# Optimization experiments

Measured on AMD Instinct MI355X. Metric: run time of the kernel, lower is better.

## Reference

```python
import jax, jax.numpy as jnp
import numpy as np

IN_D = 512
VOCAB = 32000
SEQ = 2048

def setup_inputs() -> dict:
    key = jax.random.key(0)
    ks = jax.random.split(key, 12)
    d = IN_D
    def xavier(k, shape):
        fan_in, fan_out = shape[1], shape[0]
        a = jnp.sqrt(6.0 / (fan_in + fan_out))
        return jax.random.uniform(k, shape, jnp.float32, -a, a)
    return {
        'X': jax.random.randint(ks[0], (1, SEQ), 0, VOCAB),
        'wz': xavier(ks[1], (VOCAB, d)),
        'uz': xavier(ks[2], (d, d)),
        'w': xavier(ks[3], (VOCAB, d)),
        'u': xavier(ks[4], (d, d)),
        'wr': xavier(ks[5], (VOCAB, d)),
        'ur': xavier(ks[6], (d, d)),
        'wy': xavier(ks[7], (VOCAB, d)),
        'bz': xavier(ks[8], (1, d)),
        'br': xavier(ks[9], (1, d)),
        'bh': xavier(ks[10], (1, d)),
        'by': xavier(ks[11], (1, VOCAB)),
    }

def reference(X, wz, uz, w, u, wr, ur, wy, bz, br, bh, by):
    idx = X[0]                      # (T,) batch is hardcoded to 1 in original
    ez = wz[idx]                    # (T, d) per-step embedding gathers, done once
    er = wr[idx]
    eh = w[idx]

    def step(h, emb):
        e_z, e_r, e_h = emb
        z = jax.nn.sigmoid(e_z + h @ uz.T + bz[0])
        r = jax.nn.sigmoid(e_r + h @ ur.T + br[0])
        h_xh = jnp.tanh(e_h + (r * h) @ u.T + bh[0])
        h_new = h * z + (1.0 - z) * h_xh
        return h_new, h_new

    h0 = jnp.zeros((wz.shape[1],), dtype=wz.dtype)
    _, hs = jax.lax.scan(step, h0, (ez, er, eh))   # hs: (T, d)
    logits = hs @ wy.T + by[0]                     # (T, vocab)
    outs = jax.nn.log_softmax(logits, axis=-1)     # matches squeeze(0)
    hiddens = hs[None, :, :]                       # (1, T, d)
    return outs, hiddens
```

## Files before the change

### kernel.cpp

```cpp
#include <hip/hip_runtime.h>
#include <math.h>

typedef unsigned short u16;
typedef unsigned long long u64;
typedef unsigned short us8 __attribute__((ext_vector_type(8)));
typedef short bf16x8 __attribute__((ext_vector_type(8)));
typedef float f32x4 __attribute__((ext_vector_type(4)));

#define D       512
#define SEQ     2048
#define VOCAB   32000
#define NB      16
#define RPB     32
#define STPB    512
#define PBSTR   576
#define PBTOT   (2 * NB * PBSTR)

__device__ __forceinline__ u16 f2bf(float f) {
    union { float f; unsigned i; } x; x.f = f;
    unsigned r = x.i + 0x7fff + ((x.i >> 16) & 1);
    return (u16)(r >> 16);
}

__device__ __forceinline__ u64 tag_ld(const u64* p) {
    return __hip_atomic_load(p, __ATOMIC_RELAXED, __HIP_MEMORY_SCOPE_AGENT);
}
__device__ __forceinline__ void tag_st(u64* p, u64 v) {
    __hip_atomic_store(p, v, __ATOMIC_RELAXED, __HIP_MEMORY_SCOPE_AGENT);
}
__device__ __forceinline__ u64 packtv(float f, unsigned tag) {
    union { float f; unsigned i; } x; x.f = f;
    return ((u64)tag << 32) | (u64)x.i;
}
__device__ __forceinline__ float unpackv(u64 v) {
    union { unsigned i; float f; } x; x.i = (unsigned)v;
    return x.f;
}
__device__ __forceinline__ float ftanh(float x) {
    return 1.f - 2.f / (1.f + __expf(2.f * x));
}
__device__ __forceinline__ void bar_lds() {
    asm volatile("s_waitcnt lgkmcnt(0)" ::: "memory");
    __builtin_amdgcn_s_barrier();
}

__global__ void init_scratch(u64* __restrict__ pbuf)
{
    const int t = blockIdx.x * blockDim.x + threadIdx.x;
    if (t < PBTOT) pbuf[t] = 0ull;
}

__global__ __launch_bounds__(STPB, 2) void scan_kernel(
    const int* __restrict__ X,
    const float* __restrict__ WZ, const float* __restrict__ UZ,
    const float* __restrict__ W,  const float* __restrict__ U,
    const float* __restrict__ WR, const float* __restrict__ UR,
    const float* __restrict__ BZ, const float* __restrict__ BR,
    const float* __restrict__ BH,
    u64* __restrict__ pbuf,
    float* __restrict__ outH)
{
    __shared__ int   idxsm[SEQ];
    __shared__ float hsm[(D / 32) * 33];
    __shared__ float rhsm[RPB];

    const int tid = threadIdx.x, b = blockIdx.x;
    const int r  = tid >> 4;
    const int cg = tid & 15;
    const int c0 = cg * 32;
    const int g  = b * RPB + r;
    const int i  = tid;

    for (int k = tid; k < SEQ; k += STPB) idxsm[k] = X[k];

    float uzw[32], urw[32], ucol[32];
#pragma unroll
    for (int j = 0; j < 32; j += 4) {
        f32x4 vz = *(const f32x4*)&UZ[(size_t)g * D + c0 + j];
        f32x4 vr = *(const f32x4*)&UR[(size_t)g * D + c0 + j];
        f32x4 vu = *(const f32x4*)&U [(size_t)i * D + b * RPB + j];
#pragma unroll
        for (int q = 0; q < 4; ++q) {
            uzw[j + q]  = vz[q];
            urw[j + q]  = vr[q];
            ucol[j + q] = vu[q];
        }
    }
    const float bzv = BZ[g], brv = BR[g], bhv = BH[i];

    hsm[(i >> 5) * 33 + (i & 31)] = 0.f;
    __syncthreads();

    const int i0 = idxsm[0];
    float ezc = WZ[(size_t)i0 * D + g];
    float erc = WR[(size_t)i0 * D + g];
    float ehc = W [(size_t)i0 * D + i];

    float hprev = 0.f;
    u64* const pb0 = pbuf;
    u64* const pb1 = pbuf + NB * PBSTR;

#pragma unroll 1
    for (int t = 0; t < SEQ; ++t) {
        if (t > 0 && (i >> 5) == b) outH[(size_t)(t - 1) * D + i] = hprev;

        const int tn = (t + 1 < SEQ) ? t + 1 : t;
        const int in_ = idxsm[tn];
        const float pz = WZ[(size_t)in_ * D + g];
        const float pr = WR[(size_t)in_ * D + g];
        const float ph = W [(size_t)in_ * D + i];
        const unsigned tt = (unsigned)t + 1u;
        u64* const pb = (tt & 1u) ? pb1 : pb0;

        float az = 0.f, ar = 0.f;
#pragma unroll
        for (int j = 0; j < 32; ++j) {
            float hj = hsm[cg * 33 + j];
            az = fmaf(uzw[j], hj, az);
            ar = fmaf(urw[j], hj, ar);
        }
#pragma unroll
        for (int mk = 8; mk; mk >>= 1) {
            az += __shfl_xor(az, mk);
            ar += __shfl_xor(ar, mk);
        }
        const float hrow = hsm[b * 33 + r];
        const float zz = 1.f / (1.f + __expf(-(ezc + az + bzv)));
        const float rr = 1.f / (1.f + __expf(-(erc + ar + brv)));
        if (cg == 0) rhsm[r] = rr * hrow;
        bar_lds();

        float P = 0.f;
#pragma unroll
        for (int jl = 0; jl < 32; ++jl) P = fmaf(ucol[jl], rhsm[jl], P);
        tag_st(&pb[b * PBSTR + i], packtv(P, tt));
        if (cg == 0) {
            tag_st(&pb[b * PBSTR + 512 + r], packtv(zz * hrow, tt));
            tag_st(&pb[b * PBSTR + 544 + r], packtv(1.f - zz, tt));
        }

        u64 vP[NB], vzh, voz;
        const int ow = i >> 5, il = i & 31;
        for (;;) {
            bool ok = true;
#pragma unroll
            for (int bb = 0; bb < NB; ++bb) {
                vP[bb] = tag_ld(&pb[bb * PBSTR + i]);
                ok &= ((unsigned)(vP[bb] >> 32) >= tt);
            }
            vzh = tag_ld(&pb[ow * PBSTR + 512 + il]);
            voz = tag_ld(&pb[ow * PBSTR + 544 + il]);
            ok &= ((unsigned)(vzh >> 32) >= tt) & ((unsigned)(voz >> 32) >= tt);
            if (ok) break;
        }
        float s = 0.f;
#pragma unroll
        for (int bb = 0; bb < NB; ++bb) s += unpackv(vP[bb]);
        const float hxh  = ftanh(ehc + s + bhv);
        const float hnew = unpackv(vzh) + unpackv(voz) * hxh;

        hsm[(i >> 5) * 33 + (i & 31)] = hnew;
        hprev = hnew;
        bar_lds();

        ezc = pz; erc = pr; ehc = ph;
    }
    if ((i >> 5) == b) outH[(size_t)(SEQ - 1) * D + i] = hprev;
}

#define GBM 128
#define GBN 128
#define GBK 64

__global__ __launch_bounds__(256) void gemm_logits(
    const float* __restrict__ A,
    const float* __restrict__ B,
    const float* __restrict__ BY,
    float* __restrict__ C)
{
    __shared__ __align__(16) u16 As[GBM * GBK];
    __shared__ __align__(16) u16 Bs[GBN * GBK];

    const int tid = threadIdx.x;
    const int wv = tid >> 6, lane = tid & 63;
    const int lr = lane & 15, lg = lane >> 4;
    const int bm = blockIdx.y, bn = blockIdx.x;
    const int wm = (wv >> 1) * 64, wn = (wv & 1) * 64;

    const int srow = tid >> 3;
    const int scol = (tid & 7) * 8;

    f32x4 acc[4][4] = {};

    for (int kt = 0; kt < D; kt += GBK) {
        __syncthreads();
#pragma unroll
        for (int p = 0; p < 4; ++p) {
            const int row = p * 32 + srow;
            f32x4 a0 = *(const f32x4*)&A[(size_t)(bm * GBM + row) * D + kt + scol];
            f32x4 a1 = *(const f32x4*)&A[(size_t)(bm * GBM + row) * D + kt + scol + 4];
            f32x4 b0 = *(const f32x4*)&B[(size_t)(bn * GBN + row) * D + kt + scol];
            f32x4 b1 = *(const f32x4*)&B[(size_t)(bn * GBN + row) * D + kt + scol + 4];
            us8 oa, ob;
#pragma unroll
            for (int q = 0; q < 4; ++q) {
                oa[q] = f2bf(a0[q]); oa[4 + q] = f2bf(a1[q]);
                ob[q] = f2bf(b0[q]); ob[4 + q] = f2bf(b1[q]);
            }
            *(us8*)&As[row * GBK + scol] = oa;
            *(us8*)&Bs[row * GBK + scol] = ob;
        }
        __syncthreads();
#pragma unroll
        for (int kk = 0; kk < 2; ++kk) {
            bf16x8 af[4], bfr[4];
#pragma unroll
            for (int mi = 0; mi < 4; ++mi)
                af[mi] = *(const bf16x8*)&As[(wm + mi * 16 + lr) * GBK + kk * 32 + lg * 8];
#pragma unroll
            for (int ni = 0; ni < 4; ++ni)
                bfr[ni] = *(const bf16x8*)&Bs[(wn + ni * 16 + lr) * GBK + kk * 32 + lg * 8];
#pragma unroll
            for (int mi = 0; mi < 4; ++mi)
#pragma unroll
                for (int ni = 0; ni < 4; ++ni)
                    acc[mi][ni] = __builtin_amdgcn_mfma_f32_16x16x32_bf16(
                        af[mi], bfr[ni], acc[mi][ni], 0, 0, 0);
        }
    }

#pragma unroll
    for (int ni = 0; ni < 4; ++ni) {
        const int n = bn * GBN + wn + ni * 16 + lr;
        const float byv = BY[n];
#pragma unroll
        for (int mi = 0; mi < 4; ++mi) {
#pragma unroll
            for (int q = 0; q < 4; ++q) {
                const int m = bm * GBM + wm + mi * 16 + lg * 4 + q;
                C[(size_t)m * VOCAB + n] = acc[mi][ni][q] + byv;
            }
        }
    }
}

__global__ __launch_bounds__(256) void logsoftmax_kernel(float* __restrict__ C)
{
    const int m = blockIdx.x;
    float* row = C + (size_t)m * VOCAB;
    const int tid = threadIdx.x;

    float s = 0.f;
    for (int v = tid; v < VOCAB / 4; v += 256) {
        f32x4 x = *(const f32x4*)&row[v * 4];
        s += __expf(x[0]) + __expf(x[1]) + __expf(x[2]) + __expf(x[3]);
    }
#pragma unroll
    for (int mk = 32; mk; mk >>= 1) s += __shfl_xor(s, mk);
    __shared__ float red[4];
    if ((tid & 63) == 0) red[tid >> 6] = s;
    __syncthreads();
    const float lse = __logf(red[0] + red[1] + red[2] + red[3]);

    for (int v = tid; v < VOCAB / 4; v += 256) {
        f32x4 x = *(const f32x4*)&row[v * 4];
        x[0] -= lse; x[1] -= lse; x[2] -= lse; x[3] -= lse;
        *(f32x4*)&row[v * 4] = x;
    }
}

extern "C" void kernel_launch(void* const* d_in, const int* in_sizes, int n_in,
                              void* d_out, int out_size, void* d_ws, size_t ws_size,
                              hipStream_t stream)
{
    const int*   X  = (const int*)d_in[0];
    const float* wz = (const float*)d_in[1];
    const float* uz = (const float*)d_in[2];
    const float* w  = (const float*)d_in[3];
    const float* u  = (const float*)d_in[4];
    const float* wr = (const float*)d_in[5];
    const float* ur = (const float*)d_in[6];
    const float* wy = (const float*)d_in[7];
    const float* bz = (const float*)d_in[8];
    const float* br = (const float*)d_in[9];
    const float* bh = (const float*)d_in[10];
    const float* by = (const float*)d_in[11];

    float* out  = (float*)d_out;
    float* outH = out + (size_t)SEQ * VOCAB;

    const size_t pbytes = (size_t)PBTOT * 8;
    u64* pbuf = (ws_size >= pbytes) ? (u64*)d_ws : (u64*)d_out;

    init_scratch<<<(PBTOT + STPB - 1) / STPB, STPB, 0, stream>>>(pbuf);

    scan_kernel<<<NB, STPB, 0, stream>>>(X, wz, uz, w, u, wr, ur, bz, br, bh,
                                         pbuf, outH);

    dim3 ggrid(VOCAB / GBN, SEQ / GBM);
    gemm_logits<<<ggrid, 256, 0, stream>>>(outH, wy, by, out);

    logsoftmax_kernel<<<SEQ, 256, 0, stream>>>(out);
}
```

Measured before the change: 7.261 ms.

## Reduce GRU scan partials via fixed-point atomic adds with arrival counter

```diff
diff --git a/kernel.cpp b/kernel.cpp
--- a/kernel.cpp
+++ b/kernel.cpp
@@ -3,6 +3,7 @@
 
 typedef unsigned short u16;
 typedef unsigned long long u64;
+typedef long long s64;
 typedef unsigned short us8 __attribute__((ext_vector_type(8)));
 typedef short bf16x8 __attribute__((ext_vector_type(8)));
 typedef float f32x4 __attribute__((ext_vector_type(4)));
@@ -13,8 +14,15 @@
 #define NB      16
 #define RPB     32
 #define STPB    512
-#define PBSTR   576
-#define PBTOT   (2 * NB * PBSTR)
+
+#define ACCN    ((size_t)SEQ * D * 4)
+#define ACCB    (ACCN * 8)
+
+#define FXSCALE 1073741824.0f
+#define BIAS1   (1ll << 51)
+#define SUMBIAS (1ll << 55)
+#define MASK56  ((1ull << 56) - 1)
+#define COUNT1  (1ull << 56)
 
 __device__ __forceinline__ u16 f2bf(float f) {
     union { float f; unsigned i; } x; x.f = f;
@@ -28,6 +36,9 @@
 __device__ __forceinline__ void tag_st(u64* p, u64 v) {
     __hip_atomic_store(p, v, __ATOMIC_RELAXED, __HIP_MEMORY_SCOPE_AGENT);
 }
+__device__ __forceinline__ void acc_add(u64* p, u64 v) {
+    (void)__hip_atomic_fetch_add(p, v, __ATOMIC_RELAXED, __HIP_MEMORY_SCOPE_AGENT);
+}
 __device__ __forceinline__ u64 packtv(float f, unsigned tag) {
     union { float f; unsigned i; } x; x.f = f;
     return ((u64)tag << 32) | (u64)x.i;
@@ -44,10 +55,12 @@
     __builtin_amdgcn_s_barrier();
 }
 
-__global__ void init_scratch(u64* __restrict__ pbuf)
-{
-    const int t = blockIdx.x * blockDim.x + threadIdx.x;
-    if (t < PBTOT) pbuf[t] = 0ull;
+__global__ void init_scratch(u64* __restrict__ acc)
+{
+    const size_t stride = (size_t)gridDim.x * blockDim.x;
+    for (size_t k = blockIdx.x * (size_t)blockDim.x + threadIdx.x; k < ACCN;
+         k += stride)
+        acc[k] = 0ull;
 }
 
 __global__ __launch_bounds__(STPB, 2) void scan_kernel(
@@ -57,7 +70,7 @@
     const float* __restrict__ WR, const float* __restrict__ UR,
     const float* __restrict__ BZ, const float* __restrict__ BR,
     const float* __restrict__ BH,
-    u64* __restrict__ pbuf,
+    u64* __restrict__ acc,
     float* __restrict__ outH)
 {
     __shared__ int   idxsm[SEQ];
@@ -96,21 +109,15 @@
     float erc = WR[(size_t)i0 * D + g];
     float ehc = W [(size_t)i0 * D + i];
 
-    float hprev = 0.f;
-    u64* const pb0 = pbuf;
-    u64* const pb1 = pbuf + NB * PBSTR;
-
 #pragma unroll 1
     for (int t = 0; t < SEQ; ++t) {
-        if (t > 0 && (i >> 5) == b) outH[(size_t)(t - 1) * D + i] = hprev;
-
         const int tn = (t + 1 < SEQ) ? t + 1 : t;
         const int in_ = idxsm[tn];
         const float pz = WZ[(size_t)in_ * D + g];
         const float pr = WR[(size_t)in_ * D + g];
         const float ph = W [(size_t)in_ * D + i];
         const unsigned tt = (unsigned)t + 1u;
-        u64* const pb = (tt & 1u) ? pb1 : pb0;
+        u64* const line = acc + ((size_t)t * D + i) * 4;
 
         float az = 0.f, ar = 0.f;
 #pragma unroll
@@ -133,39 +140,34 @@
         float P = 0.f;
 #pragma unroll
         for (int jl = 0; jl < 32; ++jl) P = fmaf(ucol[jl], rhsm[jl], P);
-        tag_st(&pb[b * PBSTR + i], packtv(P, tt));
+        acc_add(line + 0 - (size_t)i * 4 + ((size_t)i) * 4,
+                COUNT1 + (u64)(BIAS1 + (s64)(P * FXSCALE)));
         if (cg == 0) {
-            tag_st(&pb[b * PBSTR + 512 + r], packtv(zz * hrow, tt));
-            tag_st(&pb[b * PBSTR + 544 + r], packtv(1.f - zz, tt));
-        }
-
-        u64 vP[NB], vzh, voz;
-        const int ow = i >> 5, il = i & 31;
+            u64* oline = acc + ((size_t)t * D + g) * 4;
+            tag_st(oline + 1, packtv(zz * hrow, tt));
+            tag_st(oline + 2, packtv(1.f - zz, tt));
+        }
+
+        u64 v0, v1, v2;
         for (;;) {
-            bool ok = true;
-#pragma unroll
-            for (int bb = 0; bb < NB; ++bb) {
-                vP[bb] = tag_ld(&pb[bb * PBSTR + i]);
-                ok &= ((unsigned)(vP[bb] >> 32) >= tt);
-            }
-            vzh = tag_ld(&pb[ow * PBSTR + 512 + il]);
-            voz = tag_ld(&pb[ow * PBSTR + 544 + il]);
-            ok &= ((unsigned)(vzh >> 32) >= tt) & ((unsigned)(voz >> 32) >= tt);
-            if (ok) break;
-        }
-        float s = 0.f;
-#pragma unroll
-        for (int bb = 0; bb < NB; ++bb) s += unpackv(vP[bb]);
+            v0 = tag_ld(line + 0);
+            v1 = tag_ld(line + 1);
+            v2 = tag_ld(line + 2);
+            if ((v0 >> 56) == 16ull &&
+                (unsigned)(v1 >> 32) == tt && (unsigned)(v2 >> 32) == tt)
+                break;
+        }
+        const s64 fx = (s64)(v0 & MASK56) - SUMBIAS;
+        const float s = (float)fx * (1.0f / FXSCALE);
         const float hxh  = ftanh(ehc + s + bhv);
-        const float hnew = unpackv(vzh) + unpackv(voz) * hxh;
+        const float hnew = unpackv(v1) + unpackv(v2) * hxh;
 
         hsm[(i >> 5) * 33 + (i & 31)] = hnew;
-        hprev = hnew;
+        if ((i >> 5) == b) outH[(size_t)t * D + i] = hnew;
         bar_lds();
 
         ezc = pz; erc = pr; ehc = ph;
     }
-    if ((i >> 5) == b) outH[(size_t)(SEQ - 1) * D + i] = hprev;
 }
 
 #define GBM 128
@@ -289,13 +291,12 @@
     float* out  = (float*)d_out;
     float* outH = out + (size_t)SEQ * VOCAB;
 
-    const size_t pbytes = (size_t)PBTOT * 8;
-    u64* pbuf = (ws_size >= pbytes) ? (u64*)d_ws : (u64*)d_out;
-
-    init_scratch<<<(PBTOT + STPB - 1) / STPB, STPB, 0, stream>>>(pbuf);
+    u64* acc = (ws_size >= ACCB) ? (u64*)d_ws : (u64*)d_out;
+
+    init_scratch<<<2048, STPB, 0, stream>>>(acc);
 
     scan_kernel<<<NB, STPB, 0, stream>>>(X, wz, uz, w, u, wr, ur, bz, br, bh,
-                                         pbuf, outH);
+                                         acc, outH);
 
     dim3 ggrid(VOCAB / GBN, SEQ / GBM);
     gemm_logits<<<ggrid, 256, 0, stream>>>(outH, wy, by, out);
```

After: 7.013 ms. 1.04x faster.
